# Performance work log

Measured on AMD Instinct MI355X. Metric: run time of the kernel, lower is better.

## Reference

```python
import jax, jax.numpy as jnp
import numpy as np

D_MODEL = 1024
NUM_HEADS = 16
HEAD_DIM = D_MODEL // NUM_HEADS


def setup_inputs() -> dict:
    key = jax.random.key(0)
    ks = jax.random.split(key, 11)
    B, S = 2, 2048
    scale = 1.0 / np.sqrt(D_MODEL)
    inp = {
        "q": jax.random.normal(ks[0], (B, S, D_MODEL), jnp.float32),
        "k": jax.random.normal(ks[1], (B, S, D_MODEL), jnp.float32),
        "v": jax.random.normal(ks[2], (B, S, D_MODEL), jnp.float32),
        "Wq": jax.random.normal(ks[3], (D_MODEL, D_MODEL), jnp.float32) * scale,
        "bq": jnp.zeros((D_MODEL,), jnp.float32),
        "Wk": jax.random.normal(ks[4], (D_MODEL, D_MODEL), jnp.float32) * scale,
        "bk": jnp.zeros((D_MODEL,), jnp.float32),
        "Wv": jax.random.normal(ks[5], (D_MODEL, D_MODEL), jnp.float32) * scale,
        "bv": jnp.zeros((D_MODEL,), jnp.float32),
        "Wo": jax.random.normal(ks[6], (D_MODEL, D_MODEL), jnp.float32) * scale,
        "bo": jnp.zeros((D_MODEL,), jnp.float32),
    }
    return inp


def reference(q, k, v, Wq, bq, Wk, bk, Wv, bv, Wo, bo):
    B, S, _ = q.shape
    # Linear projections (torch Linear: x @ W.T + b), split into heads -> [b,h,s,d]
    def proj(x, W, b):
        y = jnp.einsum('bsm,nm->bsn', x, W) + b
        return y.reshape(B, -1, NUM_HEADS, HEAD_DIM).transpose(0, 2, 1, 3)
    qh = proj(q, Wq, bq)
    kh = proj(k, Wk, bk)
    vh = proj(v, Wv, bv)
    # NOTE: source scales by sqrt(d_model), NOT sqrt(head_dim) -- faithful quirk
    factor = jnp.sqrt(jnp.float32(D_MODEL))
    scores = jnp.einsum('bhqd,bhkd->bhqk', qh, kh) / factor
    attn = jax.nn.softmax(scores, axis=-1)
    out = jnp.einsum('bhqk,bhkd->bhqd', attn, vh)
    out = out.transpose(0, 2, 1, 3).reshape(B, S, D_MODEL)
    # out projection; dropout=0.0 (eval) is identity
    return jnp.einsum('bsm,nm->bsn', out, Wo) + bo
```

## Files before the change

kernel.cpp:

```cpp
#include <hip/hip_runtime.h>
#include <hip/hip_bf16.h>

typedef __hip_bfloat16 bf16;
typedef short short8 __attribute__((ext_vector_type(8)));
typedef short bs4 __attribute__((ext_vector_type(4)));
typedef float f32x4 __attribute__((ext_vector_type(4)));

#define MFMA_BF16(a, b, c) __builtin_amdgcn_mfma_f32_16x16x32_bf16(a, b, c, 0, 0, 0)
#define MFMA16_BF16(a, b, c) __builtin_amdgcn_mfma_f32_16x16x16bf16_1k(a, b, c, 0, 0, 0)

#define QSCALE 0.045084439f

__device__ __forceinline__ void async_copy16(const bf16* g, bf16* l) {
    __builtin_amdgcn_global_load_lds(
        (const __attribute__((address_space(1))) unsigned int*)(const void*)g,
        (__attribute__((address_space(3))) unsigned int*)(void*)l, 16, 0, 0);
}

__global__ __launch_bounds__(256) void convert_all(
    const float* __restrict__ q, const float* __restrict__ k, const float* __restrict__ v,
    const float* __restrict__ wq, const float* __restrict__ wk,
    const float* __restrict__ wv, const float* __restrict__ wo,
    bf16* __restrict__ qb, bf16* __restrict__ kb, bf16* __restrict__ vb,
    bf16* __restrict__ wqb, bf16* __restrict__ wkb, bf16* __restrict__ wvb,
    bf16* __restrict__ wob)
{
    int blk = blockIdx.x;
    const float* s; bf16* d; int rel;
    if      (blk < 1024) { s = q;  d = qb;  rel = blk; }
    else if (blk < 2048) { s = k;  d = kb;  rel = blk - 1024; }
    else if (blk < 3072) { s = v;  d = vb;  rel = blk - 2048; }
    else if (blk < 3328) { s = wq; d = wqb; rel = blk - 3072; }
    else if (blk < 3584) { s = wk; d = wkb; rel = blk - 3328; }
    else if (blk < 3840) { s = wv; d = wvb; rel = blk - 3584; }
    else                 { s = wo; d = wob; rel = blk - 3840; }
    size_t base = (size_t)rel * 1024 + threadIdx.x;
#pragma unroll
    for (int i = 0; i < 4; i++) {
        float4 f = ((const float4*)s)[base + i * 256];
        union { bf16 h[4]; uint2 u; } pk;
        pk.h[0] = (bf16)f.x; pk.h[1] = (bf16)f.y;
        pk.h[2] = (bf16)f.z; pk.h[3] = (bf16)f.w;
        ((uint2*)d)[base + i * 256] = pk.u;
    }
}

__global__ __launch_bounds__(256) void gemm_qkv(
    const bf16* __restrict__ qb, const bf16* __restrict__ kb, const bf16* __restrict__ vb,
    const bf16* __restrict__ wqb, const bf16* __restrict__ wkb, const bf16* __restrict__ wvb,
    const float* __restrict__ bq, const float* __restrict__ bk, const float* __restrict__ bv,
    bf16* __restrict__ Qp, bf16* __restrict__ Kp, bf16* __restrict__ Vt)
{
    __shared__ bf16 Al[128 * 64];
    __shared__ bf16 Bl[128 * 64];

    const int sel = blockIdx.y >> 3;
    const bf16* A; const bf16* W; const float* bias;
    if      (sel == 0) { A = qb; W = wqb; bias = bq; }
    else if (sel == 1) { A = kb; W = wkb; bias = bk; }
    else               { A = vb; W = wvb; bias = bv; }

    const int K = 1024, N = 1024;
    const int t = threadIdx.x;
    const int lane = t & 63, wave = t >> 6;
    const int ln = lane & 15, quad = lane >> 4;
    const int wm = wave >> 1, wn = wave & 1;
    const int m0 = blockIdx.x * 128, n0 = (blockIdx.y & 7) * 128;

    f32x4 acc[4][4];
#pragma unroll
    for (int i = 0; i < 4; i++)
#pragma unroll
        for (int j = 0; j < 4; j++) acc[i][j] = (f32x4){0.f, 0.f, 0.f, 0.f};

    const int lk = ln & 7;
    const int srow = t >> 3, sidx0 = t & 7;

    for (int k0 = 0; k0 < K; k0 += 64) {
        const bf16* Ab = A + (size_t)m0 * K + k0;
        const bf16* Wb = W + (size_t)n0 * K + k0;
#pragma unroll
        for (int p = 0; p < 4; p++) {
            int row = p * 32 + srow, idx = sidx0 ^ (row & 7);
            async_copy16(Ab + (size_t)row * K + idx * 8, &Al[(p * 256 + wave * 64) * 8]);
        }
#pragma unroll
        for (int p = 0; p < 4; p++) {
            int row = p * 32 + srow, idx = sidx0 ^ (row & 7);
            async_copy16(Wb + (size_t)row * K + idx * 8, &Bl[(p * 256 + wave * 64) * 8]);
        }
        __syncthreads();

#pragma unroll
        for (int kk = 0; kk < 2; kk++) {
            short8 af[4], bfr[4];
#pragma unroll
            for (int i = 0; i < 4; i++) {
                int r = wm * 64 + i * 16 + ln;
                af[i] = *(const short8*)&Al[r * 64 + (((kk << 2) | quad) ^ lk) * 8];
            }
#pragma unroll
            for (int j = 0; j < 4; j++) {
                int r = wn * 64 + j * 16 + ln;
                bfr[j] = *(const short8*)&Bl[r * 64 + (((kk << 2) | quad) ^ lk) * 8];
            }
#pragma unroll
            for (int i = 0; i < 4; i++)
#pragma unroll
                for (int j = 0; j < 4; j++)
                    acc[i][j] = MFMA_BF16(af[i], bfr[j], acc[i][j]);
        }
        __syncthreads();
    }

#pragma unroll
    for (int j = 0; j < 4; j++) {
        int c = n0 + wn * 64 + j * 16 + ln;
        float bv2 = bias[c];
        if (sel == 2) {
            int h = c >> 6, dd = c & 63;
#pragma unroll
            for (int i = 0; i < 4; i++) {
                int m = m0 + wm * 64 + i * 16 + quad * 4;
                int bb = m >> 11, s = m & 2047;
                union { bf16 h4[4]; uint2 u; } pk;
#pragma unroll
                for (int r = 0; r < 4; r++) pk.h4[r] = (bf16)(acc[i][j][r] + bv2);
                *(uint2*)&Vt[(((size_t)(bb * 16 + h)) * 64 + dd) * 2048 + s] = pk.u;
            }
        } else {
            bf16* out = (sel == 0) ? Qp : Kp;
            float scl = (sel == 0) ? QSCALE : 1.0f;
#pragma unroll
            for (int i = 0; i < 4; i++) {
                int rb = m0 + wm * 64 + i * 16 + quad * 4;
#pragma unroll
                for (int r = 0; r < 4; r++)
                    out[(size_t)(rb + r) * N + c] = (bf16)((acc[i][j][r] + bv2) * scl);
            }
        }
    }
}

__global__ __launch_bounds__(256) void gemm_fin(
    const bf16* __restrict__ A, const bf16* __restrict__ W,
    const float* __restrict__ bias, float* __restrict__ C)
{
    __shared__ bf16 Al[128 * 64];
    __shared__ bf16 Bl[64 * 64];

    const int K = 1024, N = 1024;
    const int t = threadIdx.x;
    const int lane = t & 63, wave = t >> 6;
    const int ln = lane & 15, quad = lane >> 4;
    const int wm = wave >> 1, wn = wave & 1;
    const int m0 = blockIdx.x * 128, n0 = blockIdx.y * 64;

    f32x4 acc[4][2];
#pragma unroll
    for (int i = 0; i < 4; i++)
#pragma unroll
        for (int j = 0; j < 2; j++) acc[i][j] = (f32x4){0.f, 0.f, 0.f, 0.f};

    const int lk = ln & 7;
    const int srow = t >> 3, sidx0 = t & 7;

    for (int k0 = 0; k0 < K; k0 += 64) {
        const bf16* Ab = A + (size_t)m0 * K + k0;
        const bf16* Wb = W + (size_t)n0 * K + k0;
#pragma unroll
        for (int p = 0; p < 4; p++) {
            int row = p * 32 + srow, idx = sidx0 ^ (row & 7);
            async_copy16(Ab + (size_t)row * K + idx * 8, &Al[(p * 256 + wave * 64) * 8]);
        }
#pragma unroll
        for (int p = 0; p < 2; p++) {
            int row = p * 32 + srow, idx = sidx0 ^ (row & 7);
            async_copy16(Wb + (size_t)row * K + idx * 8, &Bl[(p * 256 + wave * 64) * 8]);
        }
        __syncthreads();

#pragma unroll
        for (int kk = 0; kk < 2; kk++) {
            short8 af[4], bfr[2];
#pragma unroll
            for (int i = 0; i < 4; i++) {
                int r = wm * 64 + i * 16 + ln;
                af[i] = *(const short8*)&Al[r * 64 + (((kk << 2) | quad) ^ lk) * 8];
            }
#pragma unroll
            for (int j = 0; j < 2; j++) {
                int r = wn * 32 + j * 16 + ln;
                bfr[j] = *(const short8*)&Bl[r * 64 + (((kk << 2) | quad) ^ lk) * 8];
            }
#pragma unroll
            for (int i = 0; i < 4; i++)
#pragma unroll
                for (int j = 0; j < 2; j++)
                    acc[i][j] = MFMA_BF16(af[i], bfr[j], acc[i][j]);
        }
        __syncthreads();
    }

#pragma unroll
    for (int j = 0; j < 2; j++) {
        int c = n0 + wn * 32 + j * 16 + ln;
        float bv2 = bias[c];
#pragma unroll
        for (int i = 0; i < 4; i++) {
            int rb = m0 + wm * 64 + i * 16 + quad * 4;
#pragma unroll
            for (int r = 0; r < 4; r++)
                C[(size_t)(rb + r) * N + c] = acc[i][j][r] + bv2;
        }
    }
}

__global__ __launch_bounds__(256) void attn128q(
    const bf16* __restrict__ Q, const bf16* __restrict__ K,
    const bf16* __restrict__ V, bf16* __restrict__ O)
{
    const int S = 2048, D = 1024;
    __shared__ bf16 Kl[128 * 64];
    __shared__ bf16 Vl[64 * 128];

    const int t = threadIdx.x, lane = t & 63, wave = t >> 6;
    const int ln = lane & 15, quad = lane >> 4;
    const int h = blockIdx.x & 15, b = blockIdx.x >> 4, qt = blockIdx.y;
    const size_t kqbase = (size_t)b * S * D + (size_t)h * 64;
    const size_t vbase = ((size_t)(b * 16 + h)) * 64 * 2048;

    short8 aq[2][2];
#pragma unroll
    for (int g = 0; g < 2; g++) {
        const bf16* qp = Q + kqbase + (size_t)(qt * 128 + g * 64 + wave * 16 + ln) * D;
        aq[g][0] = *(const short8*)(qp + quad * 8);
        aq[g][1] = *(const short8*)(qp + 32 + quad * 8);
    }

    f32x4 o[2][4];
    float l[2] = {0.f, 0.f};
#pragma unroll
    for (int g = 0; g < 2; g++)
#pragma unroll
        for (int i = 0; i < 4; i++) o[g][i] = (f32x4){0.f, 0.f, 0.f, 0.f};

    const int lk = ln & 7;
    const int kof0 = ln * 64 + ((quad ^ lk) * 8);
    const int kof1 = ln * 64 + (((4 | quad) ^ lk) * 8);
    int vof[8];
#pragma unroll
    for (int nk = 0; nk < 8; nk++)
        vof[nk] = ln * 128 + (((nk * 2 + (quad >> 1)) ^ lk) * 8 + (quad & 1) * 4);

    const int krow = t >> 3, kidx = t & 7;
    const int vrow = t >> 4, vidx = t & 15;

    for (int kt = 0; kt < S / 128; kt++) {
#pragma unroll
        for (int p = 0; p < 4; p++) {
            int row = p * 32 + krow, idx = kidx ^ (row & 7);
            async_copy16(K + kqbase + (size_t)(kt * 128 + row) * D + idx * 8,
                         &Kl[(p * 256 + wave * 64) * 8]);
        }
#pragma unroll
        for (int p = 0; p < 4; p++) {
            int row = p * 16 + vrow, idx = vidx ^ (row & 7);
            async_copy16(V + vbase + (size_t)row * 2048 + kt * 128 + idx * 8,
                         &Vl[(p * 256 + wave * 64) * 8]);
        }
        __syncthreads();

#pragma unroll
        for (int nk = 0; nk < 8; nk++) {
            short8 kf0 = *(const short8*)&Kl[nk * 1024 + kof0];
            short8 kf1 = *(const short8*)&Kl[nk * 1024 + kof1];
            bs4 pa[2];
#pragma unroll
            for (int g = 0; g < 2; g++) {
                f32x4 a = (f32x4){0.f, 0.f, 0.f, 0.f};
                a = MFMA_BF16(kf0, aq[g][0], a);
                a = MFMA_BF16(kf1, aq[g][1], a);
                union { bs4 s4; bf16 hh[4]; } pk;
#pragma unroll
                for (int r = 0; r < 4; r++) {
                    float p = __builtin_amdgcn_exp2f(a[r]);
                    l[g] += p;
                    pk.hh[r] = (bf16)p;
                }
                pa[g] = pk.s4;
            }
#pragma unroll
            for (int nd = 0; nd < 4; nd++) {
                bs4 vb = *(const bs4*)&Vl[nd * 2048 + vof[nk]];
                o[0][nd] = MFMA16_BF16(pa[0], vb, o[0][nd]);
                o[1][nd] = MFMA16_BF16(pa[1], vb, o[1][nd]);
            }
        }
        __syncthreads();
    }

#pragma unroll
    for (int g = 0; g < 2; g++) {
        float lv = l[g];
        lv += __shfl_xor(lv, 16);
        lv += __shfl_xor(lv, 32);
#pragma unroll
        for (int r = 0; r < 4; r++) {
            float inv = __builtin_amdgcn_rcpf(__shfl(lv, quad * 4 + r));
            int row = qt * 128 + g * 64 + wave * 16 + quad * 4 + r;
#pragma unroll
            for (int nd = 0; nd < 4; nd++)
                O[((size_t)b * S + row) * D + h * 64 + nd * 16 + ln] =
                    (bf16)(o[g][nd][r] * inv);
        }
    }
}

extern "C" void kernel_launch(void* const* d_in, const int* in_sizes, int n_in,
                              void* d_out, int out_size, void* d_ws, size_t ws_size,
                              hipStream_t stream) {
    (void)in_sizes; (void)n_in; (void)out_size; (void)ws_size;
    const float* q  = (const float*)d_in[0];
    const float* k  = (const float*)d_in[1];
    const float* v  = (const float*)d_in[2];
    const float* Wq = (const float*)d_in[3];
    const float* bq = (const float*)d_in[4];
    const float* Wk = (const float*)d_in[5];
    const float* bk = (const float*)d_in[6];
    const float* Wv = (const float*)d_in[7];
    const float* bv = (const float*)d_in[8];
    const float* Wo = (const float*)d_in[9];
    const float* bo = (const float*)d_in[10];
    float* out = (float*)d_out;

    const int M = 4096, N = 1024;
    const size_t MN = (size_t)M * N;
    const size_t NN = (size_t)N * N;
    bf16* qb  = (bf16*)d_ws;
    bf16* kb  = qb + MN;
    bf16* vb  = kb + MN;
    bf16* wqb = vb + MN;
    bf16* wkb = wqb + NN;
    bf16* wvb = wkb + NN;
    bf16* wob = wvb + NN;
    bf16* Qp  = wob + NN;
    bf16* Kp  = Qp + MN;
    bf16* Vt  = Kp + MN;
    bf16* AO  = qb;

    dim3 blk(256);
    convert_all<<<4096, blk, 0, stream>>>(q, k, v, Wq, Wk, Wv, Wo,
                                          qb, kb, vb, wqb, wkb, wvb, wob);

    gemm_qkv<<<dim3(32, 24), blk, 0, stream>>>(qb, kb, vb, wqb, wkb, wvb,
                                               bq, bk, bv, Qp, Kp, Vt);

    attn128q<<<dim3(32, 16), blk, 0, stream>>>(Qp, Kp, Vt, AO);

    gemm_fin<<<dim3(32, 16), blk, 0, stream>>>(AO, wob, bo, out);
}
```

Baseline: 223.9 us.

## Double-buffer K/V tiles in attention with async prefetch and MFMA priority hints

The attention kernel now keeps two LDS buffers for K and V and issues the async global-to-LDS copies for the next key tile before computing the current one. It waits with explicit vmcnt counts and raw barriers in place of a full __syncthreads, so tile loads overlap the MFMA and exp work. It also interleaves the two query groups' QK MFMAs and wraps the MFMA sections in s_setprio. This doubles LDS use to 64KB per block, which may reduce occupancy, and relies on the hand-written vmcnt count matching the number of outstanding loads.

```diff
diff --git a/kernel.cpp b/kernel.cpp
--- a/kernel.cpp
+++ b/kernel.cpp
@@ -221,8 +221,8 @@
     const bf16* __restrict__ V, bf16* __restrict__ O)
 {
     const int S = 2048, D = 1024;
-    __shared__ bf16 Kl[128 * 64];
-    __shared__ bf16 Vl[64 * 128];
+    __shared__ bf16 Kl[2][128 * 64];
+    __shared__ bf16 Vl[2][64 * 128];
 
     const int t = threadIdx.x, lane = t & 63, wave = t >> 6;
     const int ln = lane & 15, quad = lane >> 4;
@@ -237,6 +237,7 @@
         aq[g][0] = *(const short8*)(qp + quad * 8);
         aq[g][1] = *(const short8*)(qp + 32 + quad * 8);
     }
+    asm volatile("" :: "v"(aq[0][0]), "v"(aq[0][1]), "v"(aq[1][0]), "v"(aq[1][1]));
 
     f32x4 o[2][4];
     float l[2] = {0.f, 0.f};
@@ -256,49 +257,77 @@
     const int krow = t >> 3, kidx = t & 7;
     const int vrow = t >> 4, vidx = t & 15;
 
+#define STAGE_KV(buf_, kt_) do {                                               \
+    _Pragma("unroll")                                                          \
+    for (int p = 0; p < 4; p++) {                                              \
+        int row = p * 32 + krow, idx = kidx ^ (row & 7);                       \
+        async_copy16(K + kqbase + (size_t)((kt_) * 128 + row) * D + idx * 8,   \
+                     &Kl[buf_][(p * 256 + wave * 64) * 8]);                    \
+    }                                                                          \
+    _Pragma("unroll")                                                          \
+    for (int p = 0; p < 4; p++) {                                              \
+        int row = p * 16 + vrow, idx = vidx ^ (row & 7);                       \
+        async_copy16(V + vbase + (size_t)row * 2048 + (kt_) * 128 + idx * 8,   \
+                     &Vl[buf_][(p * 256 + wave * 64) * 8]);                    \
+    }                                                                          \
+} while (0)
+
+    STAGE_KV(0, 0);
+
     for (int kt = 0; kt < S / 128; kt++) {
-#pragma unroll
-        for (int p = 0; p < 4; p++) {
-            int row = p * 32 + krow, idx = kidx ^ (row & 7);
-            async_copy16(K + kqbase + (size_t)(kt * 128 + row) * D + idx * 8,
-                         &Kl[(p * 256 + wave * 64) * 8]);
-        }
-#pragma unroll
-        for (int p = 0; p < 4; p++) {
-            int row = p * 16 + vrow, idx = vidx ^ (row & 7);
-            async_copy16(V + vbase + (size_t)row * 2048 + kt * 128 + idx * 8,
-                         &Vl[(p * 256 + wave * 64) * 8]);
-        }
-        __syncthreads();
+        const int cur = kt & 1;
+        if (kt < S / 128 - 1) {
+            STAGE_KV(cur ^ 1, kt + 1);
+            asm volatile("s_waitcnt vmcnt(8)" ::: "memory");
+        } else {
+            asm volatile("s_waitcnt vmcnt(0)" ::: "memory");
+        }
+        __builtin_amdgcn_s_barrier();
+
+        const bf16* Klc = Kl[cur];
+        const bf16* Vlc = Vl[cur];
 
 #pragma unroll
         for (int nk = 0; nk < 8; nk++) {
-            short8 kf0 = *(const short8*)&Kl[nk * 1024 + kof0];
-            short8 kf1 = *(const short8*)&Kl[nk * 1024 + kof1];
+            short8 kf0 = *(const short8*)&Klc[nk * 1024 + kof0];
+            short8 kf1 = *(const short8*)&Klc[nk * 1024 + kof1];
+
+            __builtin_amdgcn_s_setprio(1);
+            f32x4 a0 = (f32x4){0.f, 0.f, 0.f, 0.f};
+            f32x4 a1 = (f32x4){0.f, 0.f, 0.f, 0.f};
+            a0 = MFMA_BF16(kf0, aq[0][0], a0);
+            a1 = MFMA_BF16(kf0, aq[1][0], a1);
+            a0 = MFMA_BF16(kf1, aq[0][1], a0);
+            a1 = MFMA_BF16(kf1, aq[1][1], a1);
+            __builtin_amdgcn_s_setprio(0);
+
             bs4 pa[2];
-#pragma unroll
-            for (int g = 0; g < 2; g++) {
-                f32x4 a = (f32x4){0.f, 0.f, 0.f, 0.f};
-                a = MFMA_BF16(kf0, aq[g][0], a);
-                a = MFMA_BF16(kf1, aq[g][1], a);
-                union { bs4 s4; bf16 hh[4]; } pk;
+            {
+                union { bs4 s4; bf16 hh[4]; } pk0, pk1;
 #pragma unroll
                 for (int r = 0; r < 4; r++) {
-                    float p = __builtin_amdgcn_exp2f(a[r]);
-                    l[g] += p;
-                    pk.hh[r] = (bf16)p;
+                    float p0 = __builtin_amdgcn_exp2f(a0[r]);
+                    float p1 = __builtin_amdgcn_exp2f(a1[r]);
+                    l[0] += p0; l[1] += p1;
+                    pk0.hh[r] = (bf16)p0; pk1.hh[r] = (bf16)p1;
                 }
-                pa[g] = pk.s4;
-            }
+                pa[0] = pk0.s4; pa[1] = pk1.s4;
+            }
+
+            __builtin_amdgcn_s_setprio(1);
 #pragma unroll
             for (int nd = 0; nd < 4; nd++) {
-                bs4 vb = *(const bs4*)&Vl[nd * 2048 + vof[nk]];
+                bs4 vb = *(const bs4*)&Vlc[nd * 2048 + vof[nk]];
                 o[0][nd] = MFMA16_BF16(pa[0], vb, o[0][nd]);
                 o[1][nd] = MFMA16_BF16(pa[1], vb, o[1][nd]);
             }
-        }
-        __syncthreads();
-    }
+            __builtin_amdgcn_s_setprio(0);
+        }
+
+        asm volatile("" ::: "memory");
+        __builtin_amdgcn_s_barrier();
+    }
+#undef STAGE_KV
 
 #pragma unroll
     for (int g = 0; g < 2; g++) {
```

New measurement: 225.4 us. Within noise of the previous version (+0.7%).
